# Kernel optimization log

Measured on AMD Instinct MI355X. Metric: run time of the kernel, lower is better.

The kernel has to match this reference:

```python
import jax, jax.numpy as jnp
import numpy as np

D_MODEL = 1024
N_HEADS = 16
D_HEAD = D_MODEL // N_HEADS
D_FF = 4096
EPS = 1e-5


def layernorm(x, gamma, beta):
    mu = jnp.mean(x, axis=-1, keepdims=True)
    var = jnp.var(x, axis=-1, keepdims=True)
    return (x - mu) * jax.lax.rsqrt(var + EPS) * gamma + beta


def setup_inputs() -> dict:
    key = jax.random.key(0)
    ks = jax.random.split(key, 16)
    B, T = 4, 2048
    s = 1.0 / np.sqrt(D_MODEL)
    sf = 1.0 / np.sqrt(D_FF)
    return {
        "x": jax.random.normal(ks[0], (B, T, D_MODEL), jnp.float32),
        "gate_score": jax.random.uniform(ks[1], (B,), jnp.float32),
        "Wq": jax.random.normal(ks[2], (D_MODEL, D_MODEL), jnp.float32) * s,
        "bq": jnp.zeros((D_MODEL,), jnp.float32),
        "Wk": jax.random.normal(ks[3], (D_MODEL, D_MODEL), jnp.float32) * s,
        "bk": jnp.zeros((D_MODEL,), jnp.float32),
        "Wv": jax.random.normal(ks[4], (D_MODEL, D_MODEL), jnp.float32) * s,
        "bv": jnp.zeros((D_MODEL,), jnp.float32),
        "Wo": jax.random.normal(ks[5], (D_MODEL, D_MODEL), jnp.float32) * s,
        "bo": jnp.zeros((D_MODEL,), jnp.float32),
        "W1": jax.random.normal(ks[6], (D_MODEL, D_FF), jnp.float32) * s,
        "b1": jnp.zeros((D_FF,), jnp.float32),
        "W2": jax.random.normal(ks[7], (D_FF, D_MODEL), jnp.float32) * sf,
        "b2": jnp.zeros((D_MODEL,), jnp.float32),
        "gamma1": jnp.ones((D_MODEL,), jnp.float32),
        "beta1": jnp.zeros((D_MODEL,), jnp.float32),
        "gamma2": jnp.ones((D_MODEL,), jnp.float32),
        "beta2": jnp.zeros((D_MODEL,), jnp.float32),
    }


def reference(x, gate_score, Wq, bq, Wk, bk, Wv, bv, Wo, bo,
              W1, b1, W2, b2, gamma1, beta1, gamma2, beta2):
    B, T, C = x.shape
    # --- attention sub-block (pre-norm) ---
    h = layernorm(x, gamma1, beta1)
    Q = (h @ Wq + bq).reshape(B, T, N_HEADS, D_HEAD).transpose(0, 2, 1, 3)
    K = (h @ Wk + bk).reshape(B, T, N_HEADS, D_HEAD).transpose(0, 2, 1, 3)
    V = (h @ Wv + bv).reshape(B, T, N_HEADS, D_HEAD).transpose(0, 2, 1, 3)
    scores = jnp.einsum("bhqd,bhkd->bhqk", Q, K) / np.sqrt(D_HEAD)
    causal = jnp.tril(jnp.ones((T, T), dtype=bool))  # True = keep
    scores = jnp.where(causal, scores, -jnp.inf)
    attn = jax.nn.softmax(scores, axis=-1)
    ctx = jnp.einsum("bhqk,bhkd->bhqd", attn, V)
    ctx = ctx.transpose(0, 2, 1, 3).reshape(B, T, C)
    attn_out = ctx @ Wo + bo
    x1 = x + attn_out
    # --- FFN sub-block (pre-norm) ---
    h2 = layernorm(x1, gamma2, beta2)
    ff = jax.nn.gelu(h2 @ W1 + b1, approximate=False) @ W2 + b2
    x2 = x1 + ff
    # --- gated residual ---
    g = gate_score[:, None, None]
    return x + g * (x2 - x)
```

## Files before the change

kernel.cpp:

```cpp
#include <hip/hip_runtime.h>
#include <hip/hip_bf16.h>
#include <cmath>

typedef unsigned short u16;
typedef __attribute__((ext_vector_type(8))) short short8;
typedef __attribute__((ext_vector_type(4))) float f32x4;

#define DM 1024
#define NH 16
#define DH 64
#define DFF 4096
#define BB 4
#define TT 2048
#define MROWS (BB*TT)

__device__ __forceinline__ float bu2f(u16 u) {
    union { float f; unsigned v; } c; c.v = ((unsigned)u) << 16; return c.f;
}
__device__ __forceinline__ u16 f2bu(float f) {
    __hip_bfloat16 h = __float2bfloat16(f);
    union { __hip_bfloat16 h; u16 u; } c; c.h = h; return c.u;
}
__device__ __forceinline__ void async_copy16(const u16* g, u16* l) {
    __builtin_amdgcn_global_load_lds((const __attribute__((address_space(1))) void*)g,
                                     (__attribute__((address_space(3))) void*)l, 16, 0, 0);
}

__global__ void ln_kernel(const float* __restrict__ x, const float* __restrict__ gamma,
                          const float* __restrict__ beta, u16* __restrict__ out)
{
    int row = blockIdx.x;
    int tid = threadIdx.x;
    float4 v4 = ((const float4*)(x + (size_t)row * DM))[tid];
    float v[4] = { v4.x, v4.y, v4.z, v4.w };
    float s = v[0] + v[1] + v[2] + v[3];
    float ss = v[0]*v[0] + v[1]*v[1] + v[2]*v[2] + v[3]*v[3];
    #pragma unroll
    for (int o = 32; o > 0; o >>= 1) { s += __shfl_down(s, o); ss += __shfl_down(ss, o); }
    __shared__ float red[8];
    int w = tid >> 6;
    if ((tid & 63) == 0) { red[w] = s; red[4 + w] = ss; }
    __syncthreads();
    s  = red[0] + red[1] + red[2] + red[3];
    ss = red[4] + red[5] + red[6] + red[7];
    float mu  = s * (1.0f / DM);
    float var = ss * (1.0f / DM) - mu * mu;
    float rstd = rsqrtf(var + 1e-5f);
    float4 g4 = ((const float4*)gamma)[tid];
    float4 b4 = ((const float4*)beta)[tid];
    float g[4] = { g4.x, g4.y, g4.z, g4.w };
    float b[4] = { b4.x, b4.y, b4.z, b4.w };
    ushort4 o4;
    u16* op = (u16*)&o4;
    #pragma unroll
    for (int i = 0; i < 4; i++) op[i] = f2bu((v[i] - mu) * rstd * g[i] + b[i]);
    ((ushort4*)(out + (size_t)row * DM))[tid] = o4;
}

__global__ void transpose4_f2b(const float* __restrict__ w0, const float* __restrict__ w1,
                               const float* __restrict__ w2, const float* __restrict__ w3,
                               u16* __restrict__ outQKV, u16* __restrict__ outO)
{
    __shared__ u16 tile[32][33];
    const float* in = (blockIdx.z == 0) ? w0 : (blockIdx.z == 1) ? w1
                     : (blockIdx.z == 2) ? w2 : w3;
    u16* out = (blockIdx.z < 3) ? (outQKV + (size_t)blockIdx.z * DM * DM) : outO;
    int bx = blockIdx.x * 32;
    int by = blockIdx.y * 32;
    int tx = threadIdx.x, ty = threadIdx.y;
    #pragma unroll
    for (int i = 0; i < 32; i += 8)
        tile[ty + i][tx] = f2bu(in[(size_t)(by + ty + i) * DM + bx + tx]);
    __syncthreads();
    #pragma unroll
    for (int i = 0; i < 32; i += 8)
        out[(size_t)(bx + ty + i) * DM + by + tx] = tile[tx][ty + i];
}

__global__ void transpose_f2b(const float* __restrict__ in, u16* __restrict__ out,
                              int R, int C)
{
    __shared__ u16 tile[32][33];
    int bx = blockIdx.x * 32;
    int by = blockIdx.y * 32;
    int tx = threadIdx.x, ty = threadIdx.y;
    #pragma unroll
    for (int i = 0; i < 32; i += 8)
        tile[ty + i][tx] = f2bu(in[(size_t)(by + ty + i) * C + bx + tx]);
    __syncthreads();
    #pragma unroll
    for (int i = 0; i < 32; i += 8)
        out[(size_t)(bx + ty + i) * R + by + tx] = tile[tx][ty + i];
}

#define BM 128
#define BN 128
#define BK 64

template<int EPI>
__global__ void gemm_bt(
    const u16* __restrict__ A, const u16* __restrict__ Bt,
    const float* __restrict__ bias, const float* __restrict__ bias2,
    const float* __restrict__ bias3, void* __restrict__ Cv,
    const float* __restrict__ res, const float* __restrict__ x0,
    const float* __restrict__ gate, int M, int N, int K)
{
    __shared__ __align__(16) u16 As[BM * BK];
    __shared__ __align__(16) u16 Bs[BN * BK];
    int tid = threadIdx.x;
    int lane = tid & 63, wave = tid >> 6;
    int wm = (wave & 1) * 64, wn = (wave >> 1) * 64;
    int lm = lane & 15, quad = lane >> 4;
    size_t row0 = (size_t)blockIdx.x * BM;
    size_t col0 = (size_t)blockIdx.y * BN;

    int sr = tid >> 3;
    int scol = (((tid & 7) ^ (sr & 7)) * 8);
    const u16* Ag = A  + (row0 + sr) * (size_t)K + scol;
    const u16* Bg = Bt + (col0 + sr) * (size_t)K + scol;
    u16* Asl = As + tid * 8;
    u16* Bsl = Bs + tid * 8;

    int fc0 = ((0 * 4 + quad) ^ (lm & 7)) * 8;
    int fc1 = ((1 * 4 + quad) ^ (lm & 7)) * 8;

    f32x4 acc[4][4];
    #pragma unroll
    for (int i = 0; i < 4; i++)
        #pragma unroll
        for (int j = 0; j < 4; j++)
            acc[i][j] = (f32x4){0.f, 0.f, 0.f, 0.f};

    for (int k0 = 0; k0 < K; k0 += BK) {
        __syncthreads();
        async_copy16(Ag + k0,                  Asl);
        async_copy16(Ag + (size_t)32 * K + k0, Asl + 32 * BK);
        async_copy16(Ag + (size_t)64 * K + k0, Asl + 64 * BK);
        async_copy16(Ag + (size_t)96 * K + k0, Asl + 96 * BK);
        async_copy16(Bg + k0,                  Bsl);
        async_copy16(Bg + (size_t)32 * K + k0, Bsl + 32 * BK);
        async_copy16(Bg + (size_t)64 * K + k0, Bsl + 64 * BK);
        async_copy16(Bg + (size_t)96 * K + k0, Bsl + 96 * BK);
        __syncthreads();
        #pragma unroll
        for (int ks = 0; ks < 2; ks++) {
            int fc = ks ? fc1 : fc0;
            short8 af[4], bfr[4];
            #pragma unroll
            for (int t = 0; t < 4; t++) {
                af[t]  = *(const short8*)&As[(wm + t * 16 + lm) * BK + fc];
                bfr[t] = *(const short8*)&Bs[(wn + t * 16 + lm) * BK + fc];
            }
            #pragma unroll
            for (int mt = 0; mt < 4; mt++)
                #pragma unroll
                for (int nt = 0; nt < 4; nt++)
                    acc[mt][nt] = __builtin_amdgcn_mfma_f32_16x16x32_bf16(
                        af[mt], bfr[nt], acc[mt][nt], 0, 0, 0);
        }
    }

    u16*   C16 = (u16*)Cv;
    float* Cf  = (float*)Cv;

    const float* bb = bias;
    size_t csub = 0;
    if (EPI == 0 && bias2 != nullptr) {
        size_t cbase = col0 + wn;
        if (cbase >= 2048)      { bb = bias3; csub = 2048; }
        else if (cbase >= 1024) { bb = bias2; csub = 1024; }
    }

    #pragma unroll
    for (int mt = 0; mt < 4; mt++) {
        #pragma unroll
        for (int nt = 0; nt < 4; nt++) {
            #pragma unroll
            for (int r = 0; r < 4; r++) {
                size_t row = row0 + wm + mt * 16 + quad * 4 + r;
                size_t col = col0 + wn + nt * 16 + lm;
                size_t idx = row * (size_t)N + col;
                float v = acc[mt][nt][r] + bb[col - csub];
                if (EPI == 0) {
                    C16[idx] = f2bu(v);
                } else if (EPI == 1) {
                    Cf[idx] = v + res[idx];
                } else if (EPI == 2) {
                    v = 0.5f * v * (1.0f + erff(v * 0.70710678118f));
                    C16[idx] = f2bu(v);
                } else {
                    float xv  = x0[idx];
                    float x1v = res[idx];
                    float g   = gate[row >> 11];
                    Cf[idx] = xv + g * (x1v + v - xv);
                }
            }
        }
    }
}

#define AVS 72

__global__ __launch_bounds__(256, 4) void attn_mfma(
    const u16* __restrict__ QKV, u16* __restrict__ ctx)
{
    __shared__ __align__(16) u16 Kl[64][AVS];
    __shared__ __align__(16) u16 Vt[64][AVS];
    __shared__ __align__(16) u16 Pl[4][16][AVS];

    const int LD = 3 * DM;
    int tid = threadIdx.x, lane = tid & 63, w = tid >> 6;
    int lm = lane & 15, quad = lane >> 4;

    int bi = blockIdx.x;
    int pair = bi & 15, h = (bi >> 4) & 15, b = bi >> 8;
    int t1 = 31 - pair, t2 = pair;

    const size_t hoff = (size_t)h * DH;
    const u16* Qp = QKV + (size_t)b * TT * LD + hoff;
    const u16* Kp = Qp + DM;
    const u16* Vp = Qp + 2 * DM;

    short8 aqA[2], aqB[2];
    #pragma unroll
    for (int dc = 0; dc < 2; dc++) {
        aqA[dc] = *(const short8*)(Qp + (size_t)(t1 * 64 + w * 16 + lm) * LD + dc * 32 + quad * 8);
        aqB[dc] = *(const short8*)(Qp + (size_t)(t2 * 64 + w * 16 + lm) * LD + dc * 32 + quad * 8);
    }

    int kkey = tid & 63, kdim = (tid >> 6) * 16;
    int vkey = (tid & 31) * 2, vdim = (tid >> 5) * 8;

    const u16* kb0 = Kp + (size_t)kkey * LD + kdim;
    const u16* vb0 = Vp + (size_t)vkey * LD + vdim;
    const u16* vb1 = Vp + (size_t)(vkey + 1) * LD + vdim;

    const float sc = 0.18033688011f;
    const float FM = 24.0f;
    const short s1 = (short)0x3F80;
    const short8 ones = (short8){s1, s1, s1, s1, s1, s1, s1, s1};

    uint4 kr0 = *(const uint4*)(kb0);
    uint4 kr1 = *(const uint4*)(kb0 + 8);
    uint4 vr0 = *(const uint4*)(vb0);
    uint4 vr1 = *(const uint4*)(vb1);

    #pragma unroll
    for (int ti = 0; ti < 2; ti++) {
        int tcur = (ti == 0) ? t1 : t2;
        int nch = tcur + 1;
        int q0 = tcur * 64;
        int qw = q0 + w * 16;
        short8 a0 = (ti == 0) ? aqA[0] : aqB[0];
        short8 a1 = (ti == 0) ? aqA[1] : aqB[1];
        int qv = qw + lm;

        f32x4 o[4], o5;
        #pragma unroll
        for (int ds = 0; ds < 4; ds++) o[ds] = (f32x4){0.f, 0.f, 0.f, 0.f};
        o5 = (f32x4){0.f, 0.f, 0.f, 0.f};

        for (int c = 0; c < nch; c++) {
            int kb = c * 64;
            __syncthreads();
            *(uint4*)&Kl[kkey][kdim]     = kr0;
            *(uint4*)&Kl[kkey][kdim + 8] = kr1;
            {
                const u16* p0 = (const u16*)&vr0;
                const u16* p1 = (const u16*)&vr1;
                #pragma unroll
                for (int j = 0; j < 8; j++) {
                    ushort2 pk = { p0[j], p1[j] };
                    *(ushort2*)&Vt[vdim + j][vkey] = pk;
                }
            }
            __syncthreads();

            {
                size_t offn = (c + 1 < nch) ? (size_t)(c + 1) * 64 * LD : 0;
                kr0 = *(const uint4*)(kb0 + offn);
                kr1 = *(const uint4*)(kb0 + offn + 8);
                vr0 = *(const uint4*)(vb0 + offn);
                vr1 = *(const uint4*)(vb1 + offn);
            }

            f32x4 s[4];
            #pragma unroll
            for (int ks = 0; ks < 4; ks++) s[ks] = (f32x4){0.f, 0.f, 0.f, 0.f};
            #pragma unroll
            for (int ks = 0; ks < 4; ks++) {
                short8 k0 = *(const short8*)&Kl[ks * 16 + lm][quad * 8];
                short8 k1 = *(const short8*)&Kl[ks * 16 + lm][32 + quad * 8];
                s[ks] = __builtin_amdgcn_mfma_f32_16x16x32_bf16(k0, a0, s[ks], 0, 0, 0);
                s[ks] = __builtin_amdgcn_mfma_f32_16x16x32_bf16(k1, a1, s[ks], 0, 0, 0);
            }

            bool mz = (kb + 63 > qw);
            #pragma unroll
            for (int ks = 0; ks < 4; ks++) {
                int kbase = kb + ks * 16 + quad * 4;
                ushort4 pk;
                u16* pp = (u16*)&pk;
                #pragma unroll
                for (int r = 0; r < 4; r++) {
                    float v = s[ks][r] * sc - FM;
                    if (mz && (kbase + r > qv)) v = -INFINITY;
                    pp[r] = f2bu(exp2f(v));
                }
                *(ushort4*)&Pl[w][lm][ks * 16 + quad * 4] = pk;
            }

            #pragma unroll
            for (int kc = 0; kc < 2; kc++) {
                short8 ap = *(const short8*)&Pl[w][lm][kc * 32 + quad * 8];
                #pragma unroll
                for (int ds = 0; ds < 4; ds++) {
                    short8 bv = *(const short8*)&Vt[ds * 16 + lm][kc * 32 + quad * 8];
                    o[ds] = __builtin_amdgcn_mfma_f32_16x16x32_bf16(ap, bv, o[ds], 0, 0, 0);
                }
                o5 = __builtin_amdgcn_mfma_f32_16x16x32_bf16(ap, ones, o5, 0, 0, 0);
            }
        }

        float inv[4];
        #pragma unroll
        for (int r = 0; r < 4; r++) inv[r] = 1.0f / o5[r];
        #pragma unroll
        for (int ds = 0; ds < 4; ds++)
            #pragma unroll
            for (int r = 0; r < 4; r++) {
                size_t row = (size_t)(b * TT + qw + quad * 4 + r);
                ctx[row * DM + hoff + ds * 16 + lm] = f2bu(o[ds][r] * inv[r]);
            }
    }
}

extern "C" void kernel_launch(void* const* d_in, const int* in_sizes, int n_in,
                              void* d_out, int out_size, void* d_ws, size_t ws_size,
                              hipStream_t stream)
{
    const float* x    = (const float*)d_in[0];
    const float* gate = (const float*)d_in[1];
    const float* Wq   = (const float*)d_in[2];
    const float* bq   = (const float*)d_in[3];
    const float* Wk   = (const float*)d_in[4];
    const float* bk   = (const float*)d_in[5];
    const float* Wv   = (const float*)d_in[6];
    const float* bv   = (const float*)d_in[7];
    const float* Wo   = (const float*)d_in[8];
    const float* bo   = (const float*)d_in[9];
    const float* W1   = (const float*)d_in[10];
    const float* b1   = (const float*)d_in[11];
    const float* W2   = (const float*)d_in[12];
    const float* b2   = (const float*)d_in[13];
    const float* gamma1 = (const float*)d_in[14];
    const float* beta1  = (const float*)d_in[15];
    const float* gamma2 = (const float*)d_in[16];
    const float* beta2  = (const float*)d_in[17];
    float* out = (float*)d_out;

    char* ws = (char*)d_ws;
    const size_t MB = 1024 * 1024;
    u16* WtQKV = (u16*)(ws + 0 * MB);
    u16* WtO   = (u16*)(ws + 6 * MB);
    u16* Wt1   = (u16*)(ws + 8 * MB);
    u16* Wt2   = (u16*)(ws + 16 * MB);
    u16* h     = (u16*)(ws + 24 * MB);
    u16* ctx   = (u16*)(ws + 24 * MB);
    u16* QKVb  = (u16*)(ws + 40 * MB);
    float* x1  = (float*)(ws + 40 * MB);
    u16* h2    = (u16*)(ws + 72 * MB);
    u16* ff    = (u16*)(ws + 88 * MB);

    dim3 tb(32, 8);
    transpose4_f2b<<<dim3(32, 32, 4), tb, 0, stream>>>(Wq, Wk, Wv, Wo, WtQKV, WtO);
    transpose_f2b<<<dim3(DFF / 32, DM / 32), tb, 0, stream>>>(W1, Wt1, DM, DFF);
    transpose_f2b<<<dim3(DM / 32, DFF / 32), tb, 0, stream>>>(W2, Wt2, DFF, DM);

    ln_kernel<<<MROWS, 256, 0, stream>>>(x, gamma1, beta1, h);

    gemm_bt<0><<<dim3(MROWS / BM, 3 * DM / BN), 256, 0, stream>>>(
        h, WtQKV, bq, bk, bv, QKVb, nullptr, nullptr, nullptr, MROWS, 3 * DM, DM);

    attn_mfma<<<BB * NH * 16, 256, 0, stream>>>(QKVb, ctx);

    gemm_bt<1><<<dim3(MROWS / BM, DM / BN), 256, 0, stream>>>(
        ctx, WtO, bo, nullptr, nullptr, x1, x, nullptr, nullptr, MROWS, DM, DM);

    ln_kernel<<<MROWS, 256, 0, stream>>>(x1, gamma2, beta2, h2);

    gemm_bt<2><<<dim3(MROWS / BM, DFF / BN), 256, 0, stream>>>(
        h2, Wt1, b1, nullptr, nullptr, ff, nullptr, nullptr, nullptr, MROWS, DFF, DM);

    gemm_bt<3><<<dim3(MROWS / BM, DM / BN), 256, 0, stream>>>(
        ff, Wt2, b2, nullptr, nullptr, out, x1, x, gate, MROWS, DM, DFF);
}
```

Baseline: 538.6 us.

## Fuse paired attention tiles into one K/V pass and speed up bf16/GELU math

The attention kernel now handles both query tiles of a causal pair in a single loop over key chunks. Each K/V chunk is staged once and shared by both tiles, where before the loader ran two separate passes. bf16 conversion is replaced by a manual round-to-nearest bit trick with a packed two-value store. The exact erf GELU is replaced by a sigmoid-based tanh approximation using exp2 and a hardware reciprocal. These changes reduce LDS staging and barrier count plus conversion and transcendental cost, but they change GELU numerics slightly and raise register pressure.

```diff
diff --git a/kernel.cpp b/kernel.cpp
--- a/kernel.cpp
+++ b/kernel.cpp
@@ -18,8 +18,16 @@
     union { float f; unsigned v; } c; c.v = ((unsigned)u) << 16; return c.f;
 }
 __device__ __forceinline__ u16 f2bu(float f) {
-    __hip_bfloat16 h = __float2bfloat16(f);
-    union { __hip_bfloat16 h; u16 u; } c; c.h = h; return c.u;
+    unsigned u = __builtin_bit_cast(unsigned, f);
+    u += 0x7FFFu + ((u >> 16) & 1u);
+    return (u16)(u >> 16);
+}
+__device__ __forceinline__ unsigned pack_bf16x2(float a, float b) {
+    unsigned ua = __builtin_bit_cast(unsigned, a);
+    unsigned ub = __builtin_bit_cast(unsigned, b);
+    ua += 0x7FFFu + ((ua >> 16) & 1u);
+    ub += 0x7FFFu + ((ub >> 16) & 1u);
+    return __builtin_amdgcn_perm(ub, ua, 0x07060302u);
 }
 __device__ __forceinline__ void async_copy16(const u16* g, u16* l) {
     __builtin_amdgcn_global_load_lds((const __attribute__((address_space(1))) void*)g,
@@ -50,11 +58,12 @@
     float4 b4 = ((const float4*)beta)[tid];
     float g[4] = { g4.x, g4.y, g4.z, g4.w };
     float b[4] = { b4.x, b4.y, b4.z, b4.w };
-    ushort4 o4;
-    u16* op = (u16*)&o4;
-    #pragma unroll
-    for (int i = 0; i < 4; i++) op[i] = f2bu((v[i] - mu) * rstd * g[i] + b[i]);
-    ((ushort4*)(out + (size_t)row * DM))[tid] = o4;
+    float r0 = (v[0] - mu) * rstd * g[0] + b[0];
+    float r1 = (v[1] - mu) * rstd * g[1] + b[1];
+    float r2 = (v[2] - mu) * rstd * g[2] + b[2];
+    float r3 = (v[3] - mu) * rstd * g[3] + b[3];
+    uint2 o2 = { pack_bf16x2(r0, r1), pack_bf16x2(r2, r3) };
+    ((uint2*)(out + (size_t)row * DM))[tid] = o2;
 }
 
 __global__ void transpose4_f2b(const float* __restrict__ w0, const float* __restrict__ w1,
@@ -186,7 +195,11 @@
                 } else if (EPI == 1) {
                     Cf[idx] = v + res[idx];
                 } else if (EPI == 2) {
-                    v = 0.5f * v * (1.0f + erff(v * 0.70710678118f));
+                    float v2 = v * v;
+                    float y2 = v * fmaf(v2, 0.10294374f, 2.30211822f);
+                    float ex = exp2f(y2);
+                    float rr = __builtin_amdgcn_rcpf(ex + 1.0f);
+                    v = v - v * rr;
                     C16[idx] = f2bu(v);
                 } else {
                     float xv  = x0[idx];
@@ -206,7 +219,7 @@
 {
     __shared__ __align__(16) u16 Kl[64][AVS];
     __shared__ __align__(16) u16 Vt[64][AVS];
-    __shared__ __align__(16) u16 Pl[4][16][AVS];
+    __shared__ __align__(16) u16 Pl[4][32][AVS];
 
     const int LD = 3 * DM;
     int tid = threadIdx.x, lane = tid & 63, w = tid >> 6;
@@ -221,12 +234,13 @@
     const u16* Kp = Qp + DM;
     const u16* Vp = Qp + 2 * DM;
 
-    short8 aqA[2], aqB[2];
-    #pragma unroll
-    for (int dc = 0; dc < 2; dc++) {
-        aqA[dc] = *(const short8*)(Qp + (size_t)(t1 * 64 + w * 16 + lm) * LD + dc * 32 + quad * 8);
-        aqB[dc] = *(const short8*)(Qp + (size_t)(t2 * 64 + w * 16 + lm) * LD + dc * 32 + quad * 8);
-    }
+    int qwA = t1 * 64 + w * 16;
+    int qwB = t2 * 64 + w * 16;
+
+    short8 aA0 = *(const short8*)(Qp + (size_t)(qwA + lm) * LD + quad * 8);
+    short8 aA1 = *(const short8*)(Qp + (size_t)(qwA + lm) * LD + 32 + quad * 8);
+    short8 aB0 = *(const short8*)(Qp + (size_t)(qwB + lm) * LD + quad * 8);
+    short8 aB1 = *(const short8*)(Qp + (size_t)(qwB + lm) * LD + 32 + quad * 8);
 
     int kkey = tid & 63, kdim = (tid >> 6) * 16;
     int vkey = (tid & 31) * 2, vdim = (tid >> 5) * 8;
@@ -245,93 +259,123 @@
     uint4 vr0 = *(const uint4*)(vb0);
     uint4 vr1 = *(const uint4*)(vb1);
 
-    #pragma unroll
-    for (int ti = 0; ti < 2; ti++) {
-        int tcur = (ti == 0) ? t1 : t2;
-        int nch = tcur + 1;
-        int q0 = tcur * 64;
-        int qw = q0 + w * 16;
-        short8 a0 = (ti == 0) ? aqA[0] : aqB[0];
-        short8 a1 = (ti == 0) ? aqA[1] : aqB[1];
-        int qv = qw + lm;
-
-        f32x4 o[4], o5;
-        #pragma unroll
-        for (int ds = 0; ds < 4; ds++) o[ds] = (f32x4){0.f, 0.f, 0.f, 0.f};
-        o5 = (f32x4){0.f, 0.f, 0.f, 0.f};
-
-        for (int c = 0; c < nch; c++) {
-            int kb = c * 64;
-            __syncthreads();
-            *(uint4*)&Kl[kkey][kdim]     = kr0;
-            *(uint4*)&Kl[kkey][kdim + 8] = kr1;
-            {
-                const u16* p0 = (const u16*)&vr0;
-                const u16* p1 = (const u16*)&vr1;
-                #pragma unroll
-                for (int j = 0; j < 8; j++) {
-                    ushort2 pk = { p0[j], p1[j] };
-                    *(ushort2*)&Vt[vdim + j][vkey] = pk;
-                }
-            }
-            __syncthreads();
-
-            {
-                size_t offn = (c + 1 < nch) ? (size_t)(c + 1) * 64 * LD : 0;
-                kr0 = *(const uint4*)(kb0 + offn);
-                kr1 = *(const uint4*)(kb0 + offn + 8);
-                vr0 = *(const uint4*)(vb0 + offn);
-                vr1 = *(const uint4*)(vb1 + offn);
-            }
-
-            f32x4 s[4];
-            #pragma unroll
-            for (int ks = 0; ks < 4; ks++) s[ks] = (f32x4){0.f, 0.f, 0.f, 0.f};
-            #pragma unroll
-            for (int ks = 0; ks < 4; ks++) {
-                short8 k0 = *(const short8*)&Kl[ks * 16 + lm][quad * 8];
-                short8 k1 = *(const short8*)&Kl[ks * 16 + lm][32 + quad * 8];
-                s[ks] = __builtin_amdgcn_mfma_f32_16x16x32_bf16(k0, a0, s[ks], 0, 0, 0);
-                s[ks] = __builtin_amdgcn_mfma_f32_16x16x32_bf16(k1, a1, s[ks], 0, 0, 0);
-            }
-
-            bool mz = (kb + 63 > qw);
+    f32x4 oA[4], oB[4], o5A, o5B;
+    #pragma unroll
+    for (int ds = 0; ds < 4; ds++) {
+        oA[ds] = (f32x4){0.f, 0.f, 0.f, 0.f};
+        oB[ds] = (f32x4){0.f, 0.f, 0.f, 0.f};
+    }
+    o5A = (f32x4){0.f, 0.f, 0.f, 0.f};
+    o5B = (f32x4){0.f, 0.f, 0.f, 0.f};
+
+    int nch = t1 + 1;
+    for (int c = 0; c < nch; c++) {
+        int kb = c * 64;
+        bool doB = (c <= t2);
+        __syncthreads();
+        *(uint4*)&Kl[kkey][kdim]     = kr0;
+        *(uint4*)&Kl[kkey][kdim + 8] = kr1;
+        {
+            const u16* p0 = (const u16*)&vr0;
+            const u16* p1 = (const u16*)&vr1;
+            #pragma unroll
+            for (int j = 0; j < 8; j++) {
+                ushort2 pk = { p0[j], p1[j] };
+                *(ushort2*)&Vt[vdim + j][vkey] = pk;
+            }
+        }
+        __syncthreads();
+
+        {
+            size_t offn = (c + 1 < nch) ? (size_t)(c + 1) * 64 * LD : 0;
+            kr0 = *(const uint4*)(kb0 + offn);
+            kr1 = *(const uint4*)(kb0 + offn + 8);
+            vr0 = *(const uint4*)(vb0 + offn);
+            vr1 = *(const uint4*)(vb1 + offn);
+        }
+
+        f32x4 sA[4], sB[4];
+        #pragma unroll
+        for (int ks = 0; ks < 4; ks++) {
+            sA[ks] = (f32x4){0.f, 0.f, 0.f, 0.f};
+            sB[ks] = (f32x4){0.f, 0.f, 0.f, 0.f};
+        }
+        #pragma unroll
+        for (int ks = 0; ks < 4; ks++) {
+            short8 k0 = *(const short8*)&Kl[ks * 16 + lm][quad * 8];
+            short8 k1 = *(const short8*)&Kl[ks * 16 + lm][32 + quad * 8];
+            sA[ks] = __builtin_amdgcn_mfma_f32_16x16x32_bf16(k0, aA0, sA[ks], 0, 0, 0);
+            sA[ks] = __builtin_amdgcn_mfma_f32_16x16x32_bf16(k1, aA1, sA[ks], 0, 0, 0);
+            if (doB) {
+                sB[ks] = __builtin_amdgcn_mfma_f32_16x16x32_bf16(k0, aB0, sB[ks], 0, 0, 0);
+                sB[ks] = __builtin_amdgcn_mfma_f32_16x16x32_bf16(k1, aB1, sB[ks], 0, 0, 0);
+            }
+        }
+
+        {
+            bool mz = (kb + 63 > qwA);
+            int qv = qwA + lm;
             #pragma unroll
             for (int ks = 0; ks < 4; ks++) {
                 int kbase = kb + ks * 16 + quad * 4;
-                ushort4 pk;
-                u16* pp = (u16*)&pk;
+                float e[4];
                 #pragma unroll
                 for (int r = 0; r < 4; r++) {
-                    float v = s[ks][r] * sc - FM;
+                    float v = sA[ks][r] * sc - FM;
                     if (mz && (kbase + r > qv)) v = -INFINITY;
-                    pp[r] = f2bu(exp2f(v));
+                    e[r] = exp2f(v);
                 }
-                *(ushort4*)&Pl[w][lm][ks * 16 + quad * 4] = pk;
-            }
-
-            #pragma unroll
-            for (int kc = 0; kc < 2; kc++) {
-                short8 ap = *(const short8*)&Pl[w][lm][kc * 32 + quad * 8];
+                uint2 pk = { pack_bf16x2(e[0], e[1]), pack_bf16x2(e[2], e[3]) };
+                *(uint2*)&Pl[w][lm][ks * 16 + quad * 4] = pk;
+            }
+        }
+        if (doB) {
+            bool mz = (kb + 63 > qwB);
+            int qv = qwB + lm;
+            #pragma unroll
+            for (int ks = 0; ks < 4; ks++) {
+                int kbase = kb + ks * 16 + quad * 4;
+                float e[4];
                 #pragma unroll
-                for (int ds = 0; ds < 4; ds++) {
-                    short8 bv = *(const short8*)&Vt[ds * 16 + lm][kc * 32 + quad * 8];
-                    o[ds] = __builtin_amdgcn_mfma_f32_16x16x32_bf16(ap, bv, o[ds], 0, 0, 0);
+                for (int r = 0; r < 4; r++) {
+                    float v = sB[ks][r] * sc - FM;
+                    if (mz && (kbase + r > qv)) v = -INFINITY;
+                    e[r] = exp2f(v);
                 }
-                o5 = __builtin_amdgcn_mfma_f32_16x16x32_bf16(ap, ones, o5, 0, 0, 0);
-            }
-        }
-
-        float inv[4];
-        #pragma unroll
-        for (int r = 0; r < 4; r++) inv[r] = 1.0f / o5[r];
-        #pragma unroll
-        for (int ds = 0; ds < 4; ds++)
-            #pragma unroll
-            for (int r = 0; r < 4; r++) {
-                size_t row = (size_t)(b * TT + qw + quad * 4 + r);
-                ctx[row * DM + hoff + ds * 16 + lm] = f2bu(o[ds][r] * inv[r]);
-            }
+                uint2 pk = { pack_bf16x2(e[0], e[1]), pack_bf16x2(e[2], e[3]) };
+                *(uint2*)&Pl[w][16 + lm][ks * 16 + quad * 4] = pk;
+            }
+        }
+
+        #pragma unroll
+        for (int kc = 0; kc < 2; kc++) {
+            short8 apA = *(const short8*)&Pl[w][lm][kc * 32 + quad * 8];
+            short8 apB;
+            if (doB) apB = *(const short8*)&Pl[w][16 + lm][kc * 32 + quad * 8];
+            #pragma unroll
+            for (int ds = 0; ds < 4; ds++) {
+                short8 bv = *(const short8*)&Vt[ds * 16 + lm][kc * 32 + quad * 8];
+                oA[ds] = __builtin_amdgcn_mfma_f32_16x16x32_bf16(apA, bv, oA[ds], 0, 0, 0);
+                if (doB)
+                    oB[ds] = __builtin_amdgcn_mfma_f32_16x16x32_bf16(apB, bv, oB[ds], 0, 0, 0);
+            }
+            o5A = __builtin_amdgcn_mfma_f32_16x16x32_bf16(apA, ones, o5A, 0, 0, 0);
+            if (doB)
+                o5B = __builtin_amdgcn_mfma_f32_16x16x32_bf16(apB, ones, o5B, 0, 0, 0);
+        }
+    }
+
+    #pragma unroll
+    for (int r = 0; r < 4; r++) {
+        float invA = 1.0f / o5A[r];
+        float invB = 1.0f / o5B[r];
+        #pragma unroll
+        for (int ds = 0; ds < 4; ds++) {
+            size_t rowA = (size_t)(b * TT + qwA + quad * 4 + r);
+            size_t rowB = (size_t)(b * TT + qwB + quad * 4 + r);
+            ctx[rowA * DM + hoff + ds * 16 + lm] = f2bu(oA[ds][r] * invA);
+            ctx[rowB * DM + hoff + ds * 16 + lm] = f2bu(oB[ds][r] * invB);
+        }
     }
 }
 
```

Result: slower. 560.5 us (+4.1%).
